# Kernel optimization log

Measured on AMD Instinct MI355X. Metric: run time of the kernel, lower is better.

## Reference

```python
import jax, jax.numpy as jnp
import numpy as np

SEQ = 32
D = 32  # d_model == GRU hidden size


def _gru_scan(gates_x, w_hh, b_hh):
    """gates_x: [S, B, 3H] precomputed input projections (r,z,n order, PyTorch convention).
    Returns outputs [S, B, H]."""
    H = w_hh.shape[1]
    B = gates_x.shape[1]

    def step(h, gx):
        gh = h @ w_hh.T + b_hh  # [B, 3H]
        r = jax.nn.sigmoid(gx[:, :H] + gh[:, :H])
        z = jax.nn.sigmoid(gx[:, H:2 * H] + gh[:, H:2 * H])
        n = jnp.tanh(gx[:, 2 * H:] + r * gh[:, 2 * H:])
        h_new = (1.0 - z) * n + z * h
        return h_new, h_new

    h0 = jnp.zeros((B, H), gates_x.dtype)
    _, ys = jax.lax.scan(step, h0, gates_x)
    return ys


def setup_inputs() -> dict:
    key = jax.random.key(0)
    ks = jax.random.split(key, 16)
    s = 0.1
    inp = {
        "x": jax.random.normal(ks[0], (32768, SEQ), dtype=jnp.float32),
        # feature extractor: Linear(1,16) -> LeakyReLU -> Linear(16,32)
        "w1": jax.random.normal(ks[1], (16, 1), dtype=jnp.float32) * s,
        "b1": jax.random.normal(ks[2], (16,), dtype=jnp.float32) * s,
        "w2": jax.random.normal(ks[3], (D, 16), dtype=jnp.float32) * s,
        "b2": jax.random.normal(ks[4], (D,), dtype=jnp.float32) * s,
        # GRU forward direction (PyTorch layout: [3H, in], gates r,z,n)
        "w_ih_f": jax.random.normal(ks[5], (3 * D, D), dtype=jnp.float32) * s,
        "w_hh_f": jax.random.normal(ks[6], (3 * D, D), dtype=jnp.float32) * s,
        "b_ih_f": jax.random.normal(ks[7], (3 * D,), dtype=jnp.float32) * s,
        "b_hh_f": jax.random.normal(ks[8], (3 * D,), dtype=jnp.float32) * s,
        # GRU backward direction
        "w_ih_b": jax.random.normal(ks[9], (3 * D, D), dtype=jnp.float32) * s,
        "w_hh_b": jax.random.normal(ks[10], (3 * D, D), dtype=jnp.float32) * s,
        "b_ih_b": jax.random.normal(ks[11], (3 * D,), dtype=jnp.float32) * s,
        "b_hh_b": jax.random.normal(ks[12], (3 * D,), dtype=jnp.float32) * s,
        # decoder: Linear(2*D, 128)
        "w_dec": jax.random.normal(ks[13], (128, 2 * D), dtype=jnp.float32) * s,
        "b_dec": jax.random.normal(ks[14], (128,), dtype=jnp.float32) * s,
    }
    return inp


def reference(x, w1, b1, w2, b2,
              w_ih_f, w_hh_f, b_ih_f, b_hh_f,
              w_ih_b, w_hh_b, b_ih_b, b_hh_b,
              w_dec, b_dec):
    x = x.reshape(-1, SEQ, 1)                      # [B, S, 1]
    h = jax.nn.leaky_relu(x @ w1.T + b1, 0.01)     # [B, S, 16]
    feat = h @ w2.T + b2                           # [B, S, D]

    # forward direction
    gx_f = jnp.einsum('bsd,gd->sbg', feat, w_ih_f) + b_ih_f  # [S, B, 3D]
    out_f = _gru_scan(gx_f, w_hh_f, b_hh_f)                  # [S, B, D]

    # backward direction: scan over time-reversed input, flip outputs back
    feat_rev = feat[:, ::-1, :]
    gx_b = jnp.einsum('bsd,gd->sbg', feat_rev, w_ih_b) + b_ih_b
    out_b = _gru_scan(gx_b, w_hh_b, b_hh_b)[::-1]            # [S, B, D]

    out = jnp.concatenate([out_f, out_b], axis=-1)  # [S, B, 2D]
    pooled = out.mean(axis=0)                       # [B, 2D]
    return pooled @ w_dec.T + b_dec                 # [B, 128]
```

## Files before the change

kernel.cpp:

```cpp
#include <hip/hip_runtime.h>


#define SEQB 32
#define NH   16
#define DH   32

typedef __attribute__((ext_vector_type(4))) float f32x4;
typedef __attribute__((ext_vector_type(8))) short s16x8;
typedef __attribute__((ext_vector_type(4))) unsigned int u32x4;

#define MFMA_B16(a, b, c) __builtin_amdgcn_mfma_f32_16x16x32_bf16((a), (b), (c), 0, 0, 0)

#define NLOG2E -1.4426950408889634f
#define TWOLOG2E 2.8853900817779268f

#define OFF_AHI  0u
#define OFF_AGX  24576u
#define OFF_ADEC 36864u
#define OFF_WC   53248u
#define OFF_BC   65536u

__device__ __forceinline__ unsigned short bf16_rne(float x) {
    unsigned u = __float_as_uint(x);
    return (unsigned short)((u + 0x7fffu + ((u >> 16) & 1u)) >> 16);
}
__device__ __forceinline__ unsigned pack_hi(unsigned a, unsigned b) {
    return __builtin_amdgcn_perm(a, b, 0x07060302u);
}
__device__ __forceinline__ int kperm(int q, int e) {
    return (e < 4) ? (4 * q + e) : (4 * q + 12 + e);
}

__global__ __launch_bounds__(1024) void gru_precompute_kernel(
    const float* __restrict__ w_ih_f, const float* __restrict__ b_ih_f,
    const float* __restrict__ w_ih_b, const float* __restrict__ b_ih_b,
    const float* __restrict__ w2, const float* __restrict__ b2,
    const float* __restrict__ whh_f, const float* __restrict__ whh_b,
    const float* __restrict__ bhh_f, const float* __restrict__ bhh_b,
    const float* __restrict__ w_dec,
    unsigned char* __restrict__ ws)
{
    const int t = threadIdx.x;
    float* WC = (float*)(ws + OFF_WC);
    float* BC = (float*)(ws + OFF_BC);

    if (t < 192) {
        const int dir = t / 96, g = t % 96;
        const float* wih = dir ? w_ih_b : w_ih_f;
        const float* bih = dir ? b_ih_b : b_ih_f;
        float acc[NH];
#pragma unroll
        for (int m = 0; m < NH; ++m) acc[m] = 0.0f;
        float ab = bih[g];
        for (int d = 0; d < DH; ++d) {
            float wv = wih[g * DH + d];
            ab = fmaf(wv, b2[d], ab);
#pragma unroll
            for (int m = 0; m < NH; ++m) acc[m] = fmaf(wv, w2[d * NH + m], acc[m]);
        }
#pragma unroll
        for (int m = 0; m < NH; ++m) WC[(dir * 96 + g) * NH + m] = acc[m];
        BC[dir * 96 + g] = ab;
    }
    __syncthreads();

    if (t < 768) {
        const int dir = t / 384, r = t % 384, tt = r / 64, l = r % 64;
        const int gate = tt * 16 + (l & 15);
        const int q = l >> 4;
        const float* whh = dir ? whh_b : whh_f;
        const float* bhh = dir ? bhh_b : bhh_f;
        const float sc = (gate < 64) ? NLOG2E : 1.0f;
        unsigned short h8[8], g8[8];
#pragma unroll
        for (int e = 0; e < 8; ++e) {
            const int u = kperm(q, e);
            h8[e] = bf16_rne(whh[gate * DH + u] * sc);
            float gxv = (e < 4) ? WC[(dir * 96 + gate) * NH + 4 * q + e] : 0.0f;
            g8[e] = bf16_rne(gxv * sc);
        }
        const float bias = (BC[dir * 96 + gate] + ((gate < 64) ? bhh[gate] : 0.0f)) * sc;
        const unsigned bb = __float_as_uint(bias);
        if (q == 0) g8[4] = (unsigned short)(bb >> 16);
        if (q == 1) g8[4] = bf16_rne(bias - __uint_as_float(bb & 0xffff0000u));

        unsigned short* dh = (unsigned short*)(ws + OFF_AHI + dir * 6144u + tt * 1024u + l * 16u);
        unsigned short* dg = (unsigned short*)(ws + OFF_AGX + dir * 6144u + tt * 1024u + l * 16u);
#pragma unroll
        for (int e = 0; e < 8; ++e) { dh[e] = h8[e]; dg[e] = g8[e]; }
    }
    {
        const int kc = t / 512, r = t % 512, tt = r / 64, l = r % 64;
        const int outn = tt * 16 + (l & 15);
        const int q = l >> 4;
        unsigned short* dd = (unsigned short*)(ws + OFF_ADEC + kc * 8192u + tt * 1024u + l * 16u);
#pragma unroll
        for (int e = 0; e < 8; ++e)
            dd[e] = bf16_rne(w_dec[outn * 64 + kperm(q, e) + 32 * kc]);
    }
}

__global__ __launch_bounds__(256, 2) void gru_mfma_kernel(
    const float* __restrict__ x,
    const float* __restrict__ w1, const float* __restrict__ b1,
    const float* __restrict__ bhh_f, const float* __restrict__ bhh_b,
    const unsigned char* __restrict__ ws,
    const float* __restrict__ b_dec,
    float* __restrict__ out)
{
    const int tid = threadIdx.x;
    const int wv  = tid >> 6;
    const int l   = tid & 63;
    const int n = l & 15;
    const int q = l >> 4;
    const int rowbase = blockIdx.x * 64 + wv * 16;
    const float* xr = x + (size_t)(rowbase + n) * SEQB;

    const float4 w1q = *(const float4*)(w1 + 4 * q);
    const float4 b1q = *(const float4*)(b1 + 4 * q);

    float pFL[4], pFH[4], pBL[4], pBH[4];

#pragma unroll 1
    for (int dir = 0; dir < 2; ++dir) {
        const float* bhh = dir ? bhh_b : bhh_f;
        const unsigned char* pAhi = ws + OFF_AHI + dir * 6144u + l * 16u;
        const unsigned char* pAgx = ws + OFF_AGX + dir * 6144u + l * 16u;
        s16x8 Ahi[6], Agx[6];
#pragma unroll
        for (int tt = 0; tt < 6; ++tt) {
            Ahi[tt] = *(const s16x8*)(pAhi + tt * 1024);
            Agx[tt] = *(const s16x8*)(pAgx + tt * 1024);
        }
#pragma unroll
        for (int tt = 0; tt < 6; ++tt)
            asm volatile("" : "+v"(Ahi[tt]), "+v"(Agx[tt]));
        const float4 bn0f = *(const float4*)(bhh + 64 + 4 * q);
        const float4 bn1f = *(const float4*)(bhh + 80 + 4 * q);
        const f32x4 bhn0 = {bn0f.x, bn0f.y, bn0f.z, bn0f.w};
        const f32x4 bhn1 = {bn1f.x, bn1f.y, bn1f.z, bn1f.w};

        float hL[4] = {0, 0, 0, 0}, hH[4] = {0, 0, 0, 0};
        float pL[4] = {0, 0, 0, 0}, pH[4] = {0, 0, 0, 0};

#pragma unroll 1
        for (int blk = 0; blk < 4; ++blk) {
            const int bb = dir ? 3 - blk : blk;
            const float4 xa = *(const float4*)(xr + bb * 8);
            const float4 xb = *(const float4*)(xr + bb * 8 + 4);
            const float raw[8] = {xa.x, xa.y, xa.z, xa.w, xb.x, xb.y, xb.z, xb.w};
            float xs[8];
#pragma unroll
            for (int i = 0; i < 8; ++i) xs[i] = dir ? raw[7 - i] : raw[i];

#pragma unroll
            for (int i = 0; i < 8; ++i) {
                float t0 = fmaf(xs[i], w1q.x, b1q.x); t0 = fmaxf(t0, 0.01f * t0);
                float t1 = fmaf(xs[i], w1q.y, b1q.y); t1 = fmaxf(t1, 0.01f * t1);
                float t2 = fmaf(xs[i], w1q.z, b1q.z); t2 = fmaxf(t2, 0.01f * t2);
                float t3 = fmaf(xs[i], w1q.w, b1q.w); t3 = fmaxf(t3, 0.01f * t3);
                u32x4 ub1;
                ub1.x = pack_hi(__float_as_uint(t1), __float_as_uint(t0));
                ub1.y = pack_hi(__float_as_uint(t3), __float_as_uint(t2));
                ub1.z = 0x00003F80u;
                ub1.w = 0u;
                const s16x8 Bh1 = __builtin_bit_cast(s16x8, ub1);

                unsigned uL0 = __float_as_uint(hL[0]), uL1 = __float_as_uint(hL[1]);
                unsigned uL2 = __float_as_uint(hL[2]), uL3 = __float_as_uint(hL[3]);
                unsigned uH0 = __float_as_uint(hH[0]), uH1 = __float_as_uint(hH[1]);
                unsigned uH2 = __float_as_uint(hH[2]), uH3 = __float_as_uint(hH[3]);
                u32x4 phh;
                phh.x = pack_hi(uL1, uL0); phh.y = pack_hi(uL3, uL2);
                phh.z = pack_hi(uH1, uH0); phh.w = pack_hi(uH3, uH2);
                float lL0 = hL[0] - __uint_as_float(uL0 & 0xffff0000u);
                float lL1 = hL[1] - __uint_as_float(uL1 & 0xffff0000u);
                float lL2 = hL[2] - __uint_as_float(uL2 & 0xffff0000u);
                float lL3 = hL[3] - __uint_as_float(uL3 & 0xffff0000u);
                float lH0 = hH[0] - __uint_as_float(uH0 & 0xffff0000u);
                float lH1 = hH[1] - __uint_as_float(uH1 & 0xffff0000u);
                float lH2 = hH[2] - __uint_as_float(uH2 & 0xffff0000u);
                float lH3 = hH[3] - __uint_as_float(uH3 & 0xffff0000u);
                u32x4 phl;
                phl.x = pack_hi(__float_as_uint(lL1), __float_as_uint(lL0));
                phl.y = pack_hi(__float_as_uint(lL3), __float_as_uint(lL2));
                phl.z = pack_hi(__float_as_uint(lH1), __float_as_uint(lH0));
                phl.w = pack_hi(__float_as_uint(lH3), __float_as_uint(lH2));
                const s16x8 Bhhi = __builtin_bit_cast(s16x8, phh);
                const s16x8 Bhlo = __builtin_bit_cast(s16x8, phl);

                const f32x4 z4 = {0.0f, 0.0f, 0.0f, 0.0f};
                f32x4 a0 = MFMA_B16(Agx[0], Bh1, z4);
                a0 = MFMA_B16(Ahi[0], Bhlo, a0); a0 = MFMA_B16(Ahi[0], Bhhi, a0);
                f32x4 a1 = MFMA_B16(Agx[1], Bh1, z4);
                a1 = MFMA_B16(Ahi[1], Bhlo, a1); a1 = MFMA_B16(Ahi[1], Bhhi, a1);
                f32x4 a2 = MFMA_B16(Agx[2], Bh1, z4);
                a2 = MFMA_B16(Ahi[2], Bhlo, a2); a2 = MFMA_B16(Ahi[2], Bhhi, a2);
                f32x4 a3 = MFMA_B16(Agx[3], Bh1, z4);
                a3 = MFMA_B16(Ahi[3], Bhlo, a3); a3 = MFMA_B16(Ahi[3], Bhhi, a3);
                f32x4 x4a = MFMA_B16(Agx[4], Bh1, z4);
                f32x4 x5a = MFMA_B16(Agx[5], Bh1, z4);
                f32x4 g4 = MFMA_B16(Ahi[4], Bhlo, bhn0);
                g4 = MFMA_B16(Ahi[4], Bhhi, g4);
                f32x4 g5 = MFMA_B16(Ahi[5], Bhlo, bhn1);
                g5 = MFMA_B16(Ahi[5], Bhhi, g5);

#pragma unroll
                for (int rg = 0; rg < 4; ++rg) {
                    float rL = __builtin_amdgcn_rcpf(1.0f + __builtin_amdgcn_exp2f(a0[rg]));
                    float zL = __builtin_amdgcn_rcpf(1.0f + __builtin_amdgcn_exp2f(a2[rg]));
                    float tL = fmaf(rL, g4[rg], x4a[rg]);
                    float nL = fmaf(-2.0f, __builtin_amdgcn_rcpf(1.0f + __builtin_amdgcn_exp2f(tL * TWOLOG2E)), 1.0f);
                    hL[rg] = fmaf(zL, hL[rg] - nL, nL);
                    pL[rg] += hL[rg];

                    float rH = __builtin_amdgcn_rcpf(1.0f + __builtin_amdgcn_exp2f(a1[rg]));
                    float zH = __builtin_amdgcn_rcpf(1.0f + __builtin_amdgcn_exp2f(a3[rg]));
                    float tH = fmaf(rH, g5[rg], x5a[rg]);
                    float nH = fmaf(-2.0f, __builtin_amdgcn_rcpf(1.0f + __builtin_amdgcn_exp2f(tH * TWOLOG2E)), 1.0f);
                    hH[rg] = fmaf(zH, hH[rg] - nH, nH);
                    pH[rg] += hH[rg];
                }
            }
        }
        if (dir == 0) {
#pragma unroll
            for (int rg = 0; rg < 4; ++rg) { pFL[rg] = pL[rg]; pFH[rg] = pH[rg]; }
        } else {
#pragma unroll
            for (int rg = 0; rg < 4; ++rg) { pBL[rg] = pL[rg]; pBH[rg] = pH[rg]; }
        }
    }

    {
#pragma unroll
        for (int rg = 0; rg < 4; ++rg) {
            pFL[rg] *= 0.03125f; pFH[rg] *= 0.03125f;
            pBL[rg] *= 0.03125f; pBH[rg] *= 0.03125f;
        }
        u32x4 pfh, pfl, pbh, pbl;
        unsigned v0, v1, v2, v3;
        v0 = __float_as_uint(pFL[0]); v1 = __float_as_uint(pFL[1]);
        v2 = __float_as_uint(pFL[2]); v3 = __float_as_uint(pFL[3]);
        pfh.x = pack_hi(v1, v0); pfh.y = pack_hi(v3, v2);
        pfl.x = pack_hi(__float_as_uint(pFL[1] - __uint_as_float(v1 & 0xffff0000u)),
                        __float_as_uint(pFL[0] - __uint_as_float(v0 & 0xffff0000u)));
        pfl.y = pack_hi(__float_as_uint(pFL[3] - __uint_as_float(v3 & 0xffff0000u)),
                        __float_as_uint(pFL[2] - __uint_as_float(v2 & 0xffff0000u)));
        v0 = __float_as_uint(pFH[0]); v1 = __float_as_uint(pFH[1]);
        v2 = __float_as_uint(pFH[2]); v3 = __float_as_uint(pFH[3]);
        pfh.z = pack_hi(v1, v0); pfh.w = pack_hi(v3, v2);
        pfl.z = pack_hi(__float_as_uint(pFH[1] - __uint_as_float(v1 & 0xffff0000u)),
                        __float_as_uint(pFH[0] - __uint_as_float(v0 & 0xffff0000u)));
        pfl.w = pack_hi(__float_as_uint(pFH[3] - __uint_as_float(v3 & 0xffff0000u)),
                        __float_as_uint(pFH[2] - __uint_as_float(v2 & 0xffff0000u)));
        v0 = __float_as_uint(pBL[0]); v1 = __float_as_uint(pBL[1]);
        v2 = __float_as_uint(pBL[2]); v3 = __float_as_uint(pBL[3]);
        pbh.x = pack_hi(v1, v0); pbh.y = pack_hi(v3, v2);
        pbl.x = pack_hi(__float_as_uint(pBL[1] - __uint_as_float(v1 & 0xffff0000u)),
                        __float_as_uint(pBL[0] - __uint_as_float(v0 & 0xffff0000u)));
        pbl.y = pack_hi(__float_as_uint(pBL[3] - __uint_as_float(v3 & 0xffff0000u)),
                        __float_as_uint(pBL[2] - __uint_as_float(v2 & 0xffff0000u)));
        v0 = __float_as_uint(pBH[0]); v1 = __float_as_uint(pBH[1]);
        v2 = __float_as_uint(pBH[2]); v3 = __float_as_uint(pBH[3]);
        pbh.z = pack_hi(v1, v0); pbh.w = pack_hi(v3, v2);
        pbl.z = pack_hi(__float_as_uint(pBH[1] - __uint_as_float(v1 & 0xffff0000u)),
                        __float_as_uint(pBH[0] - __uint_as_float(v0 & 0xffff0000u)));
        pbl.w = pack_hi(__float_as_uint(pBH[3] - __uint_as_float(v3 & 0xffff0000u)),
                        __float_as_uint(pBH[2] - __uint_as_float(v2 & 0xffff0000u)));
        const s16x8 BpFh = __builtin_bit_cast(s16x8, pfh);
        const s16x8 BpFl = __builtin_bit_cast(s16x8, pfl);
        const s16x8 BpBh = __builtin_bit_cast(s16x8, pbh);
        const s16x8 BpBl = __builtin_bit_cast(s16x8, pbl);

#pragma unroll
        for (int tt = 0; tt < 8; ++tt) {
            const s16x8 A0 = *(const s16x8*)(ws + OFF_ADEC + tt * 1024u + l * 16u);
            const s16x8 A1 = *(const s16x8*)(ws + OFF_ADEC + 8192u + tt * 1024u + l * 16u);
            const float4 bd = *(const float4*)(b_dec + tt * 16 + 4 * q);
            f32x4 acc = {bd.x, bd.y, bd.z, bd.w};
            acc = MFMA_B16(A0, BpFl, acc);
            acc = MFMA_B16(A1, BpBl, acc);
            acc = MFMA_B16(A0, BpFh, acc);
            acc = MFMA_B16(A1, BpBh, acc);
            *(float4*)(out + (size_t)(rowbase + n) * 128 + tt * 16 + 4 * q) =
                make_float4(acc[0], acc[1], acc[2], acc[3]);
        }
    }
}

extern "C" void kernel_launch(void* const* d_in, const int* in_sizes, int n_in,
                              void* d_out, int out_size, void* d_ws, size_t ws_size,
                              hipStream_t stream)
{
    const float* x    = (const float*)d_in[0];
    const float* w1   = (const float*)d_in[1];
    const float* b1   = (const float*)d_in[2];
    const float* w2   = (const float*)d_in[3];
    const float* b2   = (const float*)d_in[4];
    const float* wihf = (const float*)d_in[5];
    const float* whhf = (const float*)d_in[6];
    const float* bihf = (const float*)d_in[7];
    const float* bhhf = (const float*)d_in[8];
    const float* wihb = (const float*)d_in[9];
    const float* whhb = (const float*)d_in[10];
    const float* bihb = (const float*)d_in[11];
    const float* bhhb = (const float*)d_in[12];
    const float* wdec = (const float*)d_in[13];
    const float* bdec = (const float*)d_in[14];
    float* out = (float*)d_out;
    unsigned char* ws = (unsigned char*)d_ws;

    const int B = in_sizes[0] / SEQB;
    const int grid = B / 64;

    hipLaunchKernelGGL(gru_precompute_kernel, dim3(1), dim3(1024), 0, stream,
                       wihf, bihf, wihb, bihb, w2, b2, whhf, whhb, bhhf, bhhb, wdec, ws);
    hipLaunchKernelGGL(gru_mfma_kernel, dim3(grid), dim3(256), 0, stream,
                       x, w1, b1, bhhf, bhhb, ws, bdec, out);
}
```

Measured before the change: 72.68 us.

## Fold tanh scale into weights, prefetch next x block, use packed bf16 convert

```diff
diff --git a/kernel.cpp b/kernel.cpp
--- a/kernel.cpp
+++ b/kernel.cpp
@@ -11,7 +11,7 @@
 
 #define MFMA_B16(a, b, c) __builtin_amdgcn_mfma_f32_16x16x32_bf16((a), (b), (c), 0, 0, 0)
 
-#define NLOG2E -1.4426950408889634f
+#define NLOG2E  -1.4426950408889634f
 #define TWOLOG2E 2.8853900817779268f
 
 #define OFF_AHI  0u
@@ -26,6 +26,11 @@
 }
 __device__ __forceinline__ unsigned pack_hi(unsigned a, unsigned b) {
     return __builtin_amdgcn_perm(a, b, 0x07060302u);
+}
+__device__ __forceinline__ unsigned cvt_pk_bf16(float a, float b) {
+    unsigned r;
+    asm("v_cvt_pk_bf16_f32 %0, %1, %2" : "=v"(r) : "v"(a), "v"(b));
+    return r;
 }
 __device__ __forceinline__ int kperm(int q, int e) {
     return (e < 4) ? (4 * q + e) : (4 * q + 12 + e);
@@ -70,7 +75,7 @@
         const int q = l >> 4;
         const float* whh = dir ? whh_b : whh_f;
         const float* bhh = dir ? bhh_b : bhh_f;
-        const float sc = (gate < 64) ? NLOG2E : 1.0f;
+        const float sc = (gate < 64) ? NLOG2E : TWOLOG2E;
         unsigned short h8[8], g8[8];
 #pragma unroll
         for (int e = 0; e < 8; ++e) {
@@ -137,17 +142,26 @@
             asm volatile("" : "+v"(Ahi[tt]), "+v"(Agx[tt]));
         const float4 bn0f = *(const float4*)(bhh + 64 + 4 * q);
         const float4 bn1f = *(const float4*)(bhh + 80 + 4 * q);
-        const f32x4 bhn0 = {bn0f.x, bn0f.y, bn0f.z, bn0f.w};
-        const f32x4 bhn1 = {bn1f.x, bn1f.y, bn1f.z, bn1f.w};
+        const f32x4 bhn0 = {bn0f.x * TWOLOG2E, bn0f.y * TWOLOG2E,
+                            bn0f.z * TWOLOG2E, bn0f.w * TWOLOG2E};
+        const f32x4 bhn1 = {bn1f.x * TWOLOG2E, bn1f.y * TWOLOG2E,
+                            bn1f.z * TWOLOG2E, bn1f.w * TWOLOG2E};
 
         float hL[4] = {0, 0, 0, 0}, hH[4] = {0, 0, 0, 0};
         float pL[4] = {0, 0, 0, 0}, pH[4] = {0, 0, 0, 0};
 
+        const int bb0 = dir ? 3 : 0;
+        float4 xa = *(const float4*)(xr + bb0 * 8);
+        float4 xb = *(const float4*)(xr + bb0 * 8 + 4);
+
 #pragma unroll 1
         for (int blk = 0; blk < 4; ++blk) {
-            const int bb = dir ? 3 - blk : blk;
-            const float4 xa = *(const float4*)(xr + bb * 8);
-            const float4 xb = *(const float4*)(xr + bb * 8 + 4);
+            float4 na = xa, nb = xb;
+            if (blk < 3) {
+                const int bbn = dir ? 2 - blk : blk + 1;
+                na = *(const float4*)(xr + bbn * 8);
+                nb = *(const float4*)(xr + bbn * 8 + 4);
+            }
             const float raw[8] = {xa.x, xa.y, xa.z, xa.w, xb.x, xb.y, xb.z, xb.w};
             float xs[8];
 #pragma unroll
@@ -160,8 +174,8 @@
                 float t2 = fmaf(xs[i], w1q.z, b1q.z); t2 = fmaxf(t2, 0.01f * t2);
                 float t3 = fmaf(xs[i], w1q.w, b1q.w); t3 = fmaxf(t3, 0.01f * t3);
                 u32x4 ub1;
-                ub1.x = pack_hi(__float_as_uint(t1), __float_as_uint(t0));
-                ub1.y = pack_hi(__float_as_uint(t3), __float_as_uint(t2));
+                ub1.x = cvt_pk_bf16(t0, t1);
+                ub1.y = cvt_pk_bf16(t2, t3);
                 ub1.z = 0x00003F80u;
                 ub1.w = 0u;
                 const s16x8 Bh1 = __builtin_bit_cast(s16x8, ub1);
@@ -182,10 +196,10 @@
                 float lH2 = hH[2] - __uint_as_float(uH2 & 0xffff0000u);
                 float lH3 = hH[3] - __uint_as_float(uH3 & 0xffff0000u);
                 u32x4 phl;
-                phl.x = pack_hi(__float_as_uint(lL1), __float_as_uint(lL0));
-                phl.y = pack_hi(__float_as_uint(lL3), __float_as_uint(lL2));
-                phl.z = pack_hi(__float_as_uint(lH1), __float_as_uint(lH0));
-                phl.w = pack_hi(__float_as_uint(lH3), __float_as_uint(lH2));
+                phl.x = cvt_pk_bf16(lL0, lL1);
+                phl.y = cvt_pk_bf16(lL2, lL3);
+                phl.z = cvt_pk_bf16(lH0, lH1);
+                phl.w = cvt_pk_bf16(lH2, lH3);
                 const s16x8 Bhhi = __builtin_bit_cast(s16x8, phh);
                 const s16x8 Bhlo = __builtin_bit_cast(s16x8, phl);
 
@@ -210,18 +224,19 @@
                     float rL = __builtin_amdgcn_rcpf(1.0f + __builtin_amdgcn_exp2f(a0[rg]));
                     float zL = __builtin_amdgcn_rcpf(1.0f + __builtin_amdgcn_exp2f(a2[rg]));
                     float tL = fmaf(rL, g4[rg], x4a[rg]);
-                    float nL = fmaf(-2.0f, __builtin_amdgcn_rcpf(1.0f + __builtin_amdgcn_exp2f(tL * TWOLOG2E)), 1.0f);
+                    float nL = fmaf(-2.0f, __builtin_amdgcn_rcpf(1.0f + __builtin_amdgcn_exp2f(tL)), 1.0f);
                     hL[rg] = fmaf(zL, hL[rg] - nL, nL);
                     pL[rg] += hL[rg];
 
                     float rH = __builtin_amdgcn_rcpf(1.0f + __builtin_amdgcn_exp2f(a1[rg]));
                     float zH = __builtin_amdgcn_rcpf(1.0f + __builtin_amdgcn_exp2f(a3[rg]));
                     float tH = fmaf(rH, g5[rg], x5a[rg]);
-                    float nH = fmaf(-2.0f, __builtin_amdgcn_rcpf(1.0f + __builtin_amdgcn_exp2f(tH * TWOLOG2E)), 1.0f);
+                    float nH = fmaf(-2.0f, __builtin_amdgcn_rcpf(1.0f + __builtin_amdgcn_exp2f(tH)), 1.0f);
                     hH[rg] = fmaf(zH, hH[rg] - nH, nH);
                     pH[rg] += hH[rg];
                 }
             }
+            xa = na; xb = nb;
         }
         if (dir == 0) {
 #pragma unroll
@@ -243,31 +258,31 @@
         v0 = __float_as_uint(pFL[0]); v1 = __float_as_uint(pFL[1]);
         v2 = __float_as_uint(pFL[2]); v3 = __float_as_uint(pFL[3]);
         pfh.x = pack_hi(v1, v0); pfh.y = pack_hi(v3, v2);
-        pfl.x = pack_hi(__float_as_uint(pFL[1] - __uint_as_float(v1 & 0xffff0000u)),
-                        __float_as_uint(pFL[0] - __uint_as_float(v0 & 0xffff0000u)));
-        pfl.y = pack_hi(__float_as_uint(pFL[3] - __uint_as_float(v3 & 0xffff0000u)),
-                        __float_as_uint(pFL[2] - __uint_as_float(v2 & 0xffff0000u)));
+        pfl.x = cvt_pk_bf16(pFL[0] - __uint_as_float(v0 & 0xffff0000u),
+                            pFL[1] - __uint_as_float(v1 & 0xffff0000u));
+        pfl.y = cvt_pk_bf16(pFL[2] - __uint_as_float(v2 & 0xffff0000u),
+                            pFL[3] - __uint_as_float(v3 & 0xffff0000u));
         v0 = __float_as_uint(pFH[0]); v1 = __float_as_uint(pFH[1]);
         v2 = __float_as_uint(pFH[2]); v3 = __float_as_uint(pFH[3]);
         pfh.z = pack_hi(v1, v0); pfh.w = pack_hi(v3, v2);
-        pfl.z = pack_hi(__float_as_uint(pFH[1] - __uint_as_float(v1 & 0xffff0000u)),
-                        __float_as_uint(pFH[0] - __uint_as_float(v0 & 0xffff0000u)));
-        pfl.w = pack_hi(__float_as_uint(pFH[3] - __uint_as_float(v3 & 0xffff0000u)),
-                        __float_as_uint(pFH[2] - __uint_as_float(v2 & 0xffff0000u)));
+        pfl.z = cvt_pk_bf16(pFH[0] - __uint_as_float(v0 & 0xffff0000u),
+                            pFH[1] - __uint_as_float(v1 & 0xffff0000u));
+        pfl.w = cvt_pk_bf16(pFH[2] - __uint_as_float(v2 & 0xffff0000u),
+                            pFH[3] - __uint_as_float(v3 & 0xffff0000u));
         v0 = __float_as_uint(pBL[0]); v1 = __float_as_uint(pBL[1]);
         v2 = __float_as_uint(pBL[2]); v3 = __float_as_uint(pBL[3]);
         pbh.x = pack_hi(v1, v0); pbh.y = pack_hi(v3, v2);
-        pbl.x = pack_hi(__float_as_uint(pBL[1] - __uint_as_float(v1 & 0xffff0000u)),
-                        __float_as_uint(pBL[0] - __uint_as_float(v0 & 0xffff0000u)));
-        pbl.y = pack_hi(__float_as_uint(pBL[3] - __uint_as_float(v3 & 0xffff0000u)),
-                        __float_as_uint(pBL[2] - __uint_as_float(v2 & 0xffff0000u)));
+        pbl.x = cvt_pk_bf16(pBL[0] - __uint_as_float(v0 & 0xffff0000u),
+                            pBL[1] - __uint_as_float(v1 & 0xffff0000u));
+        pbl.y = cvt_pk_bf16(pBL[2] - __uint_as_float(v2 & 0xffff0000u),
+                            pBL[3] - __uint_as_float(v3 & 0xffff0000u));
         v0 = __float_as_uint(pBH[0]); v1 = __float_as_uint(pBH[1]);
         v2 = __float_as_uint(pBH[2]); v3 = __float_as_uint(pBH[3]);
         pbh.z = pack_hi(v1, v0); pbh.w = pack_hi(v3, v2);
-        pbl.z = pack_hi(__float_as_uint(pBH[1] - __uint_as_float(v1 & 0xffff0000u)),
-                        __float_as_uint(pBH[0] - __uint_as_float(v0 & 0xffff0000u)));
-        pbl.w = pack_hi(__float_as_uint(pBH[3] - __uint_as_float(v3 & 0xffff0000u)),
-                        __float_as_uint(pBH[2] - __uint_as_float(v2 & 0xffff0000u)));
+        pbl.z = cvt_pk_bf16(pBH[0] - __uint_as_float(v0 & 0xffff0000u),
+                            pBH[1] - __uint_as_float(v1 & 0xffff0000u));
+        pbl.w = cvt_pk_bf16(pBH[2] - __uint_as_float(v2 & 0xffff0000u),
+                            pBH[3] - __uint_as_float(v3 & 0xffff0000u));
         const s16x8 BpFh = __builtin_bit_cast(s16x8, pfh);
         const s16x8 BpFl = __builtin_bit_cast(s16x8, pfl);
         const s16x8 BpBh = __builtin_bit_cast(s16x8, pbh);
```

Measured after the change: 73.08 us. No clear change (+0.5%).
